# Performance work log

Hardware: AMD Instinct MI355X
Metric: run time of the kernel (lower is better)

Reference implementation:

```python
import jax, jax.numpy as jnp
import numpy as np


def _consts():
    # Hypercube vertices: itertools.product([-1,1], repeat=n) order => MSB-first bits.
    def verts(nbits):
        idx = np.arange(2 ** nbits)
        return (((idx[:, None] >> np.arange(nbits - 1, -1, -1)[None, :]) & 1) * 2.0 - 1.0).astype(np.float32)

    hexagrams = verts(6)   # (64, 6)
    q2_verts = verts(2)    # (4, 2)
    q3_verts = verts(3)    # (8, 3)

    # Q2 vertex -> group one-hot, _Q2_TO_GROUP = [2, 1, 1, 0]
    q2_to_group = np.zeros((4, 3), dtype=np.float32)
    for v, g in enumerate([2, 1, 1, 0]):
        q2_to_group[v, g] = 1.0

    # Group anchors: ABSTRACT = mean(hex[63], hex[62]), DYNAMIC = mean(hex[19], hex[21]),
    # CONCRETE = mean(hex[0], hex[8]); then L2-normalized.
    anch = np.stack([
        hexagrams[[63, 62]].mean(0),
        hexagrams[[19, 21]].mean(0),
        hexagrams[[0, 8]].mean(0),
    ]).astype(np.float32)
    anch = anch / np.clip(np.linalg.norm(anch, axis=-1, keepdims=True), 1e-12, None)

    # Walsh-Hadamard popcount masks, pre-divided by their sums -> (64, 3) matrix.
    bits = np.array([bin(i).count('1') for i in range(64)], dtype=np.float32)
    wa = (bits >= 5).astype(np.float32)
    wd = (bits == 3).astype(np.float32)
    wc = (bits <= 1).astype(np.float32)
    wht_mat = np.stack([wa / wa.sum(), wd / wd.sum(), wc / wc.sum()], axis=1)

    return tuple(jnp.asarray(a) for a in (hexagrams, q2_verts, q3_verts, q2_to_group, anch, wht_mat))


def _q3_to_group_init():
    q3_map = np.zeros((8, 3), dtype=np.float32)
    for i in range(8):
        yc = bin(i).count('1')
        if yc == 0:
            q3_map[i, 2] = 1.0
        elif yc == 1:
            q3_map[i, 1] = 1.0
        elif yc == 2:
            q3_map[i, 0] = 0.6
            q3_map[i, 1] = 0.4
        else:
            q3_map[i, 0] = 1.0
    q3_map = q3_map / np.clip(q3_map.sum(axis=1, keepdims=True), 1e-8, None)
    return q3_map


def setup_inputs() -> dict:
    key = jax.random.key(0)
    k_x, k2, k3, k6 = jax.random.split(key, 4)
    B, T, D = 4, 4096, 2048
    s = 1.0 / float(np.sqrt(D))  # torch Linear default init range
    return {
        'x': jax.random.normal(k_x, (B, T, D), dtype=jnp.float32),
        'ln_w': jnp.ones((D,), dtype=jnp.float32),
        'ln_b': jnp.zeros((D,), dtype=jnp.float32),
        'w_q2': jax.random.uniform(k2, (2, D), minval=-s, maxval=s, dtype=jnp.float32),
        'w_q3': jax.random.uniform(k3, (3, D), minval=-s, maxval=s, dtype=jnp.float32),
        'w_q6': jax.random.uniform(k6, (6, D), minval=-s, maxval=s, dtype=jnp.float32),
        'log_temp': jnp.asarray(np.log(0.5), dtype=jnp.float32),
        'log_scale_mix': jnp.zeros((3,), dtype=jnp.float32),
        'q3_to_group': jnp.asarray(_q3_to_group_init()),
        'log_wht_mix': jnp.asarray(-2.0, dtype=jnp.float32),
    }


def _forward(x, ln_w, ln_b, w_q2, w_q3, w_q6, log_temp, log_scale_mix, q3_to_group, log_wht_mix):
    hexa, q2v, q3v, q2g, anch, wht_mat = _consts()

    # LayerNorm (eps = 1e-5, torch default)
    mu = x.mean(-1, keepdims=True)
    var = ((x - mu) ** 2).mean(-1, keepdims=True)
    h = (x - mu) * jax.lax.rsqrt(var + 1e-5) * ln_w + ln_b

    temp = jnp.clip(jnp.exp(log_temp), 0.1, 5.0)

    # Q2 scale: (B,T,2) -> 4 vertices -> 3 groups
    w2 = jax.nn.softmax(jnp.tanh(h @ w_q2.T) @ q2v.T / temp, axis=-1)
    score_q2 = w2 @ q2g

    # Q3 scale: (B,T,3) -> 8 vertices -> learned soft group map
    w3 = jax.nn.softmax(jnp.tanh(h @ w_q3.T) @ q3v.T / temp, axis=-1)
    score_q3 = w3 @ jax.nn.softmax(q3_to_group, axis=-1)

    # Q6 scale: (B,T,6) -> 64 hexagram vertices
    hex_w = jax.nn.softmax(jnp.tanh(h @ w_q6.T) @ hexa.T / temp, axis=-1)
    score_cos = (hex_w @ hexa) @ anch.T            # cosine-sim vs normalized anchors
    score_wht = hex_w @ wht_mat                    # popcount-mask averages
    alpha = jax.nn.sigmoid(log_wht_mix)
    score_q6 = (1.0 - alpha) * score_cos + alpha * score_wht

    mix = jax.nn.softmax(log_scale_mix)
    group_w = jax.nn.softmax(mix[0] * score_q2 + mix[1] * score_q3 + mix[2] * score_q6, axis=-1)

    mg = group_w.mean(axis=(0, 1))
    mh = hex_w.mean(axis=(0, 1))
    lb_loss = jnp.sum(mg * jnp.log(mg + 1e-8)) + 0.1 * jnp.sum(mh * jnp.log(mh + 1e-8))
    return group_w, hex_w, lb_loss


def reference(x, ln_w, ln_b, w_q2, w_q3, w_q6, log_temp, log_scale_mix, q3_to_group, log_wht_mix):
    return _forward(x, ln_w, ln_b, w_q2, w_q3, w_q6, log_temp, log_scale_mix, q3_to_group, log_wht_mix)
```

## Files before the change

kernel.cpp:

```cpp
#include <hip/hip_runtime.h>
#include <math.h>
#include <string.h>

#define D 2048
#define NTOK 16384
#define NROW 11
#define MROWS_U32 (NROW * D / 2)
#define K1_BLOCKS 1024
#define K1_THREADS 256
#define WSTRIDE_U 1036
#define TILE_S 20

#define WS_A 0
#define WS_B 16
#define WS_IT 32
#define WS_ALPHA 33
#define WS_MIX 34
#define WS_M3 40
#define WS_MERGED 64
#define WS_PART (WS_MERGED + MROWS_U32)

typedef __fp16 h2 __attribute__((ext_vector_type(2)));
typedef __fp16 h8 __attribute__((ext_vector_type(8)));
typedef float f32x4 __attribute__((ext_vector_type(4)));

__device__ __forceinline__ float wsum(float v){
#pragma unroll
  for (int m = 1; m < 64; m <<= 1) v += __shfl_xor(v, m, 64);
  return v;
}
__device__ __forceinline__ float wmax(float v){
#pragma unroll
  for (int m = 1; m < 64; m <<= 1) v = fmaxf(v, __shfl_xor(v, m, 64));
  return v;
}
__device__ __forceinline__ float rcp_fast(float x){ return __builtin_amdgcn_rcpf(x); }
__device__ __forceinline__ float tanh_fast(float x){
  float e = __expf(2.0f * x);
  return 1.0f - 2.0f * rcp_fast(e + 1.0f);
}
__device__ __forceinline__ float sload(const float* __restrict__ p){
  return __uint_as_float(__builtin_amdgcn_readfirstlane(__float_as_uint(*p)));
}
__device__ __forceinline__ unsigned int h2u(h2 h){ unsigned int u; memcpy(&u, &h, 4); return u; }

__global__ __launch_bounds__(256) void k0_prep(
    const float* __restrict__ ln_w, const float* __restrict__ ln_b,
    const float* __restrict__ w_q2, const float* __restrict__ w_q3,
    const float* __restrict__ w_q6,
    const float* __restrict__ log_temp, const float* __restrict__ log_scale_mix,
    const float* __restrict__ q3_to_group, const float* __restrict__ log_wht_mix,
    float* __restrict__ ws)
{
  const int tid = threadIdx.x;
  const int k = blockIdx.x;
  unsigned int* wsu = (unsigned int*)ws;
  if (k < NROW){
    const float* row = (k < 2) ? (w_q2 + (size_t)k * D)
                     : (k < 5) ? (w_q3 + (size_t)(k - 2) * D)
                               : (w_q6 + (size_t)(k - 5) * D);
    float pa = 0.f, pb = 0.f;
    for (int i = tid * 2; i < D; i += 512){
      float w0 = row[i], w1 = row[i + 1];
      h2 h = __builtin_amdgcn_cvt_pkrtz(ln_w[i] * w0, ln_w[i + 1] * w1);
      pa += (float)h[0] + (float)h[1];
      pb = fmaf(ln_b[i], w0, pb);
      pb = fmaf(ln_b[i + 1], w1, pb);
      wsu[WS_MERGED + k * 1024 + i / 2] = h2u(h);
    }
    __shared__ float red[8];
    pa = wsum(pa); pb = wsum(pb);
    if ((tid & 63) == 0){ red[tid >> 6] = pa; red[4 + (tid >> 6)] = pb; }
    __syncthreads();
    if (tid == 0){
      ws[WS_A + k] = red[0] + red[1] + red[2] + red[3];
      ws[WS_B + k] = red[4] + red[5] + red[6] + red[7];
    }
  } else if (tid < 64){
    const int lane = tid;
    float q3v = (lane < 24) ? q3_to_group[lane]   : 0.f;
    float sc  = (lane < 3)  ? log_scale_mix[lane] : 0.f;
    float lt  = (lane == 0) ? log_temp[0]         : 0.f;
    float lw  = (lane == 0) ? log_wht_mix[0]      : 0.f;

    if (lane == 0){
      float t = __expf(lt);
      t = fminf(fmaxf(t, 0.1f), 5.0f);
      ws[WS_IT] = 1.0f / t;
      ws[WS_ALPHA] = 1.0f / (1.0f + __expf(-lw));
    }
    float m0 = __shfl(sc, 0, 64), m1 = __shfl(sc, 1, 64), m2 = __shfl(sc, 2, 64);
    if (lane < 3){
      float mm = fmaxf(m0, fmaxf(m1, m2));
      float e0 = __expf(m0 - mm), e1 = __expf(m1 - mm), e2 = __expf(m2 - mm);
      float inv = 1.0f / (e0 + e1 + e2);
      ws[WS_MIX + lane] = ((lane == 0) ? e0 : (lane == 1) ? e1 : e2) * inv;
    }
    if (lane < 24){
      int r = lane / 3, c = lane - r * 3;
      float v0 = __shfl(q3v, r*3 + 0, 64);
      float v1 = __shfl(q3v, r*3 + 1, 64);
      float v2 = __shfl(q3v, r*3 + 2, 64);
      float mx = fmaxf(v0, fmaxf(v1, v2));
      float f0 = __expf(v0 - mx), f1 = __expf(v1 - mx), f2 = __expf(v2 - mx);
      float iv = 1.0f / (f0 + f1 + f2);
      ws[WS_M3 + lane] = ((c == 0) ? f0 : (c == 1) ? f1 : f2) * iv;
    }
  }
}

__global__ __launch_bounds__(256) void k1_main(
    const float* __restrict__ x, const float* __restrict__ ws,
    float* __restrict__ gout, float* __restrict__ hout, float* __restrict__ part)
{
  __shared__ unsigned int sW[NROW * WSTRIDE_U];
  __shared__ float tile[4][16][TILE_S];
  __shared__ float lred[4][68];
  const int tid  = threadIdx.x;
  const int lane = tid & 63;
  const int wid  = tid >> 6;
  const int blk  = blockIdx.x;
  const int tok0 = blk * 16;
  const int n = lane & 15;
  const int q = lane >> 4;

  const float* xp = x + (size_t)(tok0 + n) * D + wid * 512 + q * 8;

  float4 xa[16];
#pragma unroll
  for (int s = 0; s < 8; ++s){
    xa[2*s]     = *(const float4*)(xp + s * 32);
    xa[2*s + 1] = *(const float4*)(xp + s * 32 + 4);
  }

  {
    const uint4* src = (const uint4*)((const unsigned int*)ws + WS_MERGED);
#pragma unroll
    for (int j = 0; j < 11; ++j){
      int idx = tid + j * 256;
      int r = idx >> 8, i = idx & 255;
      *(uint4*)(sW + r * WSTRIDE_U + i * 4) = src[r * 256 + i];
    }
  }

  float sq = 0.f;
  h8 hxA[8], hxB[8];
#pragma unroll
  for (int s = 0; s < 8; ++s){
    float4 f0 = xa[2*s], f1 = xa[2*s + 1];
    sq = fmaf(f0.x,f0.x, fmaf(f0.y,f0.y, fmaf(f0.z,f0.z, fmaf(f0.w,f0.w, sq))));
    sq = fmaf(f1.x,f1.x, fmaf(f1.y,f1.y, fmaf(f1.z,f1.z, fmaf(f1.w,f1.w, sq))));
    h2 p0 = __builtin_amdgcn_cvt_pkrtz(f0.x, f0.y);
    h2 p1 = __builtin_amdgcn_cvt_pkrtz(f0.z, f0.w);
    h2 p2 = __builtin_amdgcn_cvt_pkrtz(f1.x, f1.y);
    h2 p3 = __builtin_amdgcn_cvt_pkrtz(f1.z, f1.w);
    h8 A;
    A[0]=p0[0]; A[1]=p0[1]; A[2]=p1[0]; A[3]=p1[1];
    A[4]=p2[0]; A[5]=p2[1]; A[6]=p3[0]; A[7]=p3[1];
    hxA[s] = A;
  }

  __syncthreads();

#pragma unroll
  for (int s = 0; s < 8; ++s){
    xa[2*s]     = *(const float4*)(xp + (s + 8) * 32);
    xa[2*s + 1] = *(const float4*)(xp + (s + 8) * 32 + 4);
  }

  const int wr = (n < NROW) ? n : (n - NROW);
  const bool is_ones = (n == NROW);
  const uint4 ones4 = make_uint4(0x3C003C00u, 0x3C003C00u, 0x3C003C00u, 0x3C003C00u);
  const unsigned int* wb = sW + wr * WSTRIDE_U + wid * 256 + q * 4;

  f32x4 acc = {0.f, 0.f, 0.f, 0.f};

#pragma unroll
  for (int s = 0; s < 8; ++s){
    uint4 wq = *(const uint4*)(wb + s * 16);
    if (is_ones) wq = ones4;
    h8 B; memcpy(&B, &wq, 16);
    acc = __builtin_amdgcn_mfma_f32_16x16x32_f16(hxA[s], B, acc, 0, 0, 0);
  }

#pragma unroll
  for (int s = 0; s < 8; ++s){
    float4 f0 = xa[2*s], f1 = xa[2*s + 1];
    sq = fmaf(f0.x,f0.x, fmaf(f0.y,f0.y, fmaf(f0.z,f0.z, fmaf(f0.w,f0.w, sq))));
    sq = fmaf(f1.x,f1.x, fmaf(f1.y,f1.y, fmaf(f1.z,f1.z, fmaf(f1.w,f1.w, sq))));
    h2 p0 = __builtin_amdgcn_cvt_pkrtz(f0.x, f0.y);
    h2 p1 = __builtin_amdgcn_cvt_pkrtz(f0.z, f0.w);
    h2 p2 = __builtin_amdgcn_cvt_pkrtz(f1.x, f1.y);
    h2 p3 = __builtin_amdgcn_cvt_pkrtz(f1.z, f1.w);
    h8 A;
    A[0]=p0[0]; A[1]=p0[1]; A[2]=p1[0]; A[3]=p1[1];
    A[4]=p2[0]; A[5]=p2[1]; A[6]=p3[0]; A[7]=p3[1];
    hxB[s] = A;
  }

#pragma unroll
  for (int s = 0; s < 8; ++s){
    uint4 wq = *(const uint4*)(wb + (s + 8) * 16);
    if (is_ones) wq = ones4;
    h8 B; memcpy(&B, &wq, 16);
    acc = __builtin_amdgcn_mfma_f32_16x16x32_f16(hxB[s], B, acc, 0, 0, 0);
  }

  sq += __shfl_xor(sq, 16, 64);
  sq += __shfl_xor(sq, 32, 64);

#pragma unroll
  for (int r = 0; r < 4; ++r) tile[wid][q * 4 + r][n] = acc[r];
  if (lane < 16) tile[wid][lane][16] = sq;

  __syncthreads();

  float a[NROW], bb[NROW];
#pragma unroll
  for (int k = 0; k < NROW; ++k){ a[k] = sload(ws + WS_A + k); bb[k] = sload(ws + WS_B + k); }
  const float it    = sload(ws + WS_IT);
  const float alpha = sload(ws + WS_ALPHA);
  const float mix0 = sload(ws + WS_MIX), mix1 = sload(ws + WS_MIX + 1), mix2 = sload(ws + WS_MIX + 2);
  float M3r[8][3];
#pragma unroll
  for (int r = 0; r < 8; ++r){
#pragma unroll
    for (int g = 0; g < 3; ++g) M3r[r][g] = sload(ws + WS_M3 + r*3 + g);
  }

  float sgn[6];
#pragma unroll
  for (int j = 0; j < 6; ++j) sgn[j] = ((lane >> (5 - j)) & 1) ? 1.0f : -1.0f;
  const float C5 = 0.44721359549995793f;
  const float A0c[6] = { C5,  C5,  C5,  C5,  C5, 0.f };
  const float A1c[6] = {-0.5f, 0.5f, -0.5f, 0.f, 0.f, 0.5f};
  const float A2c[6] = {-C5, -C5, 0.f, -C5, -C5, -C5};
  float cs0 = 0.f, cs1 = 0.f, cs2 = 0.f;
#pragma unroll
  for (int j = 0; j < 6; ++j){
    cs0 = fmaf(sgn[j], A0c[j], cs0);
    cs1 = fmaf(sgn[j], A1c[j], cs1);
    cs2 = fmaf(sgn[j], A2c[j], cs2);
  }
  const int pc = __popc(lane);
  const float w7c = 1.0f / 7.0f;
  float wh0 = (pc >= 5) ? w7c  : 0.f;
  float wh1 = (pc == 3) ? 0.05f: 0.f;
  float wh2 = (pc <= 1) ? w7c  : 0.f;
  const float m60 = (1.f - alpha)*cs0 + alpha*wh0;
  const float m61 = (1.f - alpha)*cs1 + alpha*wh1;
  const float m62 = (1.f - alpha)*cs2 + alpha*wh2;

  float hsum = 0.f, ga0 = 0.f, ga1 = 0.f, ga2 = 0.f;

#pragma unroll
  for (int i = 0; i < 4; ++i){
    const int tl  = wid * 4 + i;
    const int tok = tok0 + tl;

    float t[12]; float sqv = 0.f;
#pragma unroll
    for (int k = 0; k < 12; ++k) t[k] = 0.f;
#pragma unroll
    for (int hh = 0; hh < 4; ++hh){
      const float* row = &tile[hh][tl][0];
      float4 c0 = *(const float4*)(row);
      float4 c1 = *(const float4*)(row + 4);
      float4 c2 = *(const float4*)(row + 8);
      t[0] += c0.x; t[1] += c0.y; t[2]  += c0.z; t[3]  += c0.w;
      t[4] += c1.x; t[5] += c1.y; t[6]  += c1.z; t[7]  += c1.w;
      t[8] += c2.x; t[9] += c2.y; t[10] += c2.z; t[11] += c2.w;
      sqv += row[16];
    }

    float mean = t[11] * (1.0f / D);
    float var  = fmaf(sqv, 1.0f / D, -mean * mean);
    float rr   = rsqrtf(var + 1e-5f);
    float u[NROW];
#pragma unroll
    for (int k = 0; k < NROW; ++k){
      float d = fmaf(-mean, a[k], t[k]);
      u[k] = tanh_fast(fmaf(rr, d, bb[k]));
    }

    float p01 = u[0] + u[1], m01 = u[0] - u[1];
    float l0 = -p01*it, l1 = -m01*it, l2 = m01*it, l3 = p01*it;
    float mx2 = fmaxf(fmaxf(l0, l1), fmaxf(l2, l3));
    float e0 = __expf(l0-mx2), e1 = __expf(l1-mx2), e2 = __expf(l2-mx2), e3 = __expf(l3-mx2);
    float i2 = rcp_fast(e0 + e1 + e2 + e3);
    float s2g0 = e3 * i2, s2g1 = (e1 + e2) * i2, s2g2 = e0 * i2;

    float l3v[8]; float mx3 = -1e30f;
#pragma unroll
    for (int v = 0; v < 8; ++v){
      float acc3 = ((v & 4) ? u[2] : -u[2]) + ((v & 2) ? u[3] : -u[3]) + ((v & 1) ? u[4] : -u[4]);
      l3v[v] = acc3 * it;
      mx3 = fmaxf(mx3, l3v[v]);
    }
    float w3v[8]; float se3 = 0.f;
#pragma unroll
    for (int v = 0; v < 8; ++v){ w3v[v] = __expf(l3v[v] - mx3); se3 += w3v[v]; }
    float i3 = rcp_fast(se3);
    float s3g0 = 0.f, s3g1 = 0.f, s3g2 = 0.f;
#pragma unroll
    for (int v = 0; v < 8; ++v){
      s3g0 = fmaf(w3v[v], M3r[v][0], s3g0);
      s3g1 = fmaf(w3v[v], M3r[v][1], s3g1);
      s3g2 = fmaf(w3v[v], M3r[v][2], s3g2);
    }
    s3g0 *= i3; s3g1 *= i3; s3g2 *= i3;

    float lg = 0.f;
#pragma unroll
    for (int jj = 0; jj < 6; ++jj) lg = fmaf(sgn[jj], u[5 + jj], lg);
    lg *= it;
    float mx6 = wmax(lg);
    float p   = __expf(lg - mx6);
    float se6 = wsum(p);
    float hw  = p * rcp_fast(se6);
    hout[(size_t)tok * 64 + lane] = hw;
    hsum += hw;
    float s6g0 = wsum(hw * m60);
    float s6g1 = wsum(hw * m61);
    float s6g2 = wsum(hw * m62);

    float g0 = mix0*s2g0 + mix1*s3g0 + mix2*s6g0;
    float g1 = mix0*s2g1 + mix1*s3g1 + mix2*s6g1;
    float g2 = mix0*s2g2 + mix1*s3g2 + mix2*s6g2;
    float gm = fmaxf(g0, fmaxf(g1, g2));
    float y0 = __expf(g0-gm), y1 = __expf(g1-gm), y2 = __expf(g2-gm);
    float gi = rcp_fast(y0 + y1 + y2);
    float gw0 = y0*gi, gw1 = y1*gi, gw2 = y2*gi;
    ga0 += gw0; ga1 += gw1; ga2 += gw2;
    if (lane < 3){
      float val = (lane == 0) ? gw0 : (lane == 1) ? gw1 : gw2;
      gout[(size_t)tok * 3 + lane] = val;
    }
  }

  lred[wid][lane] = hsum;
  if (lane < 3){
    float val = (lane == 0) ? ga0 : (lane == 1) ? ga1 : ga2;
    lred[wid][64 + lane] = val;
  }
  __syncthreads();
  if (tid < 67){
    float v = lred[0][tid] + lred[1][tid] + lred[2][tid] + lred[3][tid];
    part[(size_t)tid * K1_BLOCKS + blk] = v;
  }
}

__global__ __launch_bounds__(1024) void k2_loss(const float* __restrict__ part,
                                                float* __restrict__ lout)
{
  __shared__ float sums[68];
  const int tid = threadIdx.x;
  const int lane = tid & 63;
  const int wid  = tid >> 6;
  for (int jv = wid; jv < 67; jv += 16){
    const float4* p = (const float4*)(part + (size_t)jv * K1_BLOCKS);
    float v = 0.f;
#pragma unroll
    for (int b = 0; b < K1_BLOCKS / 256; ++b){
      float4 q = p[lane + b * 64];
      v += (q.x + q.y) + (q.z + q.w);
    }
    v = wsum(v);
    if (lane == 0) sums[jv] = v;
  }
  __syncthreads();
  if (wid == 0){
    const float inv = 1.0f / (float)NTOK;
    float mh = sums[lane] * inv;
    float term = 0.1f * mh * logf(mh + 1e-8f);
    if (lane < 3){
      float mg = sums[64 + lane] * inv;
      term += mg * logf(mg + 1e-8f);
    }
    float L = wsum(term);
    if (lane == 0) lout[0] = L;
  }
}

extern "C" void kernel_launch(void* const* d_in, const int* in_sizes, int n_in,
                              void* d_out, int out_size, void* d_ws, size_t ws_size,
                              hipStream_t stream)
{
  const float* x             = (const float*)d_in[0];
  const float* ln_w          = (const float*)d_in[1];
  const float* ln_b          = (const float*)d_in[2];
  const float* w_q2          = (const float*)d_in[3];
  const float* w_q3          = (const float*)d_in[4];
  const float* w_q6          = (const float*)d_in[5];
  const float* log_temp      = (const float*)d_in[6];
  const float* log_scale_mix = (const float*)d_in[7];
  const float* q3_to_group   = (const float*)d_in[8];
  const float* log_wht_mix   = (const float*)d_in[9];

  float* out  = (float*)d_out;
  float* gout = out;
  float* hout = out + (size_t)NTOK * 3;
  float* lout = out + (size_t)NTOK * 3 + (size_t)NTOK * 64;
  float* ws   = (float*)d_ws;

  k0_prep<<<12, 256, 0, stream>>>(ln_w, ln_b, w_q2, w_q3, w_q6,
                                  log_temp, log_scale_mix, q3_to_group, log_wht_mix, ws);
  k1_main<<<K1_BLOCKS, K1_THREADS, 0, stream>>>(x, ws, gout, hout, ws + WS_PART);
  k2_loss<<<1, 1024, 0, stream>>>(ws + WS_PART, lout);
}
```

Measured before the change: 46.58 us.

## Process four tokens per wave in parallel and reduce loss partials via atomics

The epilogue now assigns each 16-lane group of a wave to one token, with each lane handling four hexagram vertices, instead of looping over four tokens with full 64-lane reductions. This replaces the serial per-token loop and its 64-wide shuffle reductions with 16-wide ones, and writes hex weights as float4. Loss partial sums are accumulated with atomicAdd into 16 striped sets, which k0 zeroes, so the final kernel shrinks to one wave. The costs are atomic contention on the sets and a dependency on k0 zeroing the accumulators before k1 runs.

```diff
diff --git a/kernel.cpp b/kernel.cpp
--- a/kernel.cpp
+++ b/kernel.cpp
@@ -10,6 +10,7 @@
 #define K1_THREADS 256
 #define WSTRIDE_U 1036
 #define TILE_S 20
+#define NSET 16
 
 #define WS_A 0
 #define WS_B 16
@@ -18,7 +19,7 @@
 #define WS_MIX 34
 #define WS_M3 40
 #define WS_MERGED 64
-#define WS_PART (WS_MERGED + MROWS_U32)
+#define WS_ACC (WS_MERGED + MROWS_U32)
 
 typedef __fp16 h2 __attribute__((ext_vector_type(2)));
 typedef __fp16 h8 __attribute__((ext_vector_type(8)));
@@ -29,9 +30,14 @@
   for (int m = 1; m < 64; m <<= 1) v += __shfl_xor(v, m, 64);
   return v;
 }
-__device__ __forceinline__ float wmax(float v){
-#pragma unroll
-  for (int m = 1; m < 64; m <<= 1) v = fmaxf(v, __shfl_xor(v, m, 64));
+__device__ __forceinline__ float gsum(float v){
+#pragma unroll
+  for (int m = 1; m < 16; m <<= 1) v += __shfl_xor(v, m, 64);
+  return v;
+}
+__device__ __forceinline__ float gmax(float v){
+#pragma unroll
+  for (int m = 1; m < 16; m <<= 1) v = fmaxf(v, __shfl_xor(v, m, 64));
   return v;
 }
 __device__ __forceinline__ float rcp_fast(float x){ return __builtin_amdgcn_rcpf(x); }
@@ -106,16 +112,19 @@
       float iv = 1.0f / (f0 + f1 + f2);
       ws[WS_M3 + lane] = ((c == 0) ? f0 : (c == 1) ? f1 : f2) * iv;
     }
+  } else {
+    for (int i = tid - 64; i < 67 * NSET; i += 192) ws[WS_ACC + i] = 0.f;
   }
 }
 
 __global__ __launch_bounds__(256) void k1_main(
     const float* __restrict__ x, const float* __restrict__ ws,
-    float* __restrict__ gout, float* __restrict__ hout, float* __restrict__ part)
+    float* __restrict__ gout, float* __restrict__ hout, float* __restrict__ accp)
 {
   __shared__ unsigned int sW[NROW * WSTRIDE_U];
   __shared__ float tile[4][16][TILE_S];
-  __shared__ float lred[4][68];
+  __shared__ float4 lredh4[4][16];
+  __shared__ float lredg[4][3];
   const int tid  = threadIdx.x;
   const int lane = tid & 63;
   const int wid  = tid >> 6;
@@ -225,161 +234,174 @@
 #pragma unroll
   for (int r = 0; r < 8; ++r){
 #pragma unroll
-    for (int g = 0; g < 3; ++g) M3r[r][g] = sload(ws + WS_M3 + r*3 + g);
-  }
-
-  float sgn[6];
-#pragma unroll
-  for (int j = 0; j < 6; ++j) sgn[j] = ((lane >> (5 - j)) & 1) ? 1.0f : -1.0f;
+    for (int g2 = 0; g2 < 3; ++g2) M3r[r][g2] = sload(ws + WS_M3 + r*3 + g2);
+  }
+
+  const int g  = lane >> 4;
+  const int l  = lane & 15;
+  const int tl  = wid * 4 + g;
+  const int tok = tok0 + tl;
+
   const float C5 = 0.44721359549995793f;
   const float A0c[6] = { C5,  C5,  C5,  C5,  C5, 0.f };
   const float A1c[6] = {-0.5f, 0.5f, -0.5f, 0.f, 0.f, 0.5f};
   const float A2c[6] = {-C5, -C5, 0.f, -C5, -C5, -C5};
-  float cs0 = 0.f, cs1 = 0.f, cs2 = 0.f;
-#pragma unroll
-  for (int j = 0; j < 6; ++j){
-    cs0 = fmaf(sgn[j], A0c[j], cs0);
-    cs1 = fmaf(sgn[j], A1c[j], cs1);
-    cs2 = fmaf(sgn[j], A2c[j], cs2);
-  }
-  const int pc = __popc(lane);
   const float w7c = 1.0f / 7.0f;
-  float wh0 = (pc >= 5) ? w7c  : 0.f;
-  float wh1 = (pc == 3) ? 0.05f: 0.f;
-  float wh2 = (pc <= 1) ? w7c  : 0.f;
-  const float m60 = (1.f - alpha)*cs0 + alpha*wh0;
-  const float m61 = (1.f - alpha)*cs1 + alpha*wh1;
-  const float m62 = (1.f - alpha)*cs2 + alpha*wh2;
-
-  float hsum = 0.f, ga0 = 0.f, ga1 = 0.f, ga2 = 0.f;
-
-#pragma unroll
-  for (int i = 0; i < 4; ++i){
-    const int tl  = wid * 4 + i;
-    const int tok = tok0 + tl;
-
-    float t[12]; float sqv = 0.f;
-#pragma unroll
-    for (int k = 0; k < 12; ++k) t[k] = 0.f;
-#pragma unroll
-    for (int hh = 0; hh < 4; ++hh){
-      const float* row = &tile[hh][tl][0];
-      float4 c0 = *(const float4*)(row);
-      float4 c1 = *(const float4*)(row + 4);
-      float4 c2 = *(const float4*)(row + 8);
-      t[0] += c0.x; t[1] += c0.y; t[2]  += c0.z; t[3]  += c0.w;
-      t[4] += c1.x; t[5] += c1.y; t[6]  += c1.z; t[7]  += c1.w;
-      t[8] += c2.x; t[9] += c2.y; t[10] += c2.z; t[11] += c2.w;
-      sqv += row[16];
-    }
-
-    float mean = t[11] * (1.0f / D);
-    float var  = fmaf(sqv, 1.0f / D, -mean * mean);
-    float rr   = rsqrtf(var + 1e-5f);
-    float u[NROW];
-#pragma unroll
-    for (int k = 0; k < NROW; ++k){
-      float d = fmaf(-mean, a[k], t[k]);
-      u[k] = tanh_fast(fmaf(rr, d, bb[k]));
-    }
-
-    float p01 = u[0] + u[1], m01 = u[0] - u[1];
-    float l0 = -p01*it, l1 = -m01*it, l2 = m01*it, l3 = p01*it;
-    float mx2 = fmaxf(fmaxf(l0, l1), fmaxf(l2, l3));
-    float e0 = __expf(l0-mx2), e1 = __expf(l1-mx2), e2 = __expf(l2-mx2), e3 = __expf(l3-mx2);
-    float i2 = rcp_fast(e0 + e1 + e2 + e3);
-    float s2g0 = e3 * i2, s2g1 = (e1 + e2) * i2, s2g2 = e0 * i2;
-
-    float l3v[8]; float mx3 = -1e30f;
-#pragma unroll
-    for (int v = 0; v < 8; ++v){
-      float acc3 = ((v & 4) ? u[2] : -u[2]) + ((v & 2) ? u[3] : -u[3]) + ((v & 1) ? u[4] : -u[4]);
-      l3v[v] = acc3 * it;
-      mx3 = fmaxf(mx3, l3v[v]);
-    }
-    float w3v[8]; float se3 = 0.f;
-#pragma unroll
-    for (int v = 0; v < 8; ++v){ w3v[v] = __expf(l3v[v] - mx3); se3 += w3v[v]; }
-    float i3 = rcp_fast(se3);
-    float s3g0 = 0.f, s3g1 = 0.f, s3g2 = 0.f;
-#pragma unroll
-    for (int v = 0; v < 8; ++v){
-      s3g0 = fmaf(w3v[v], M3r[v][0], s3g0);
-      s3g1 = fmaf(w3v[v], M3r[v][1], s3g1);
-      s3g2 = fmaf(w3v[v], M3r[v][2], s3g2);
-    }
-    s3g0 *= i3; s3g1 *= i3; s3g2 *= i3;
-
-    float lg = 0.f;
-#pragma unroll
-    for (int jj = 0; jj < 6; ++jj) lg = fmaf(sgn[jj], u[5 + jj], lg);
-    lg *= it;
-    float mx6 = wmax(lg);
-    float p   = __expf(lg - mx6);
-    float se6 = wsum(p);
-    float hw  = p * rcp_fast(se6);
-    hout[(size_t)tok * 64 + lane] = hw;
-    hsum += hw;
-    float s6g0 = wsum(hw * m60);
-    float s6g1 = wsum(hw * m61);
-    float s6g2 = wsum(hw * m62);
-
-    float g0 = mix0*s2g0 + mix1*s3g0 + mix2*s6g0;
-    float g1 = mix0*s2g1 + mix1*s3g1 + mix2*s6g1;
-    float g2 = mix0*s2g2 + mix1*s3g2 + mix2*s6g2;
-    float gm = fmaxf(g0, fmaxf(g1, g2));
-    float y0 = __expf(g0-gm), y1 = __expf(g1-gm), y2 = __expf(g2-gm);
-    float gi = rcp_fast(y0 + y1 + y2);
-    float gw0 = y0*gi, gw1 = y1*gi, gw2 = y2*gi;
-    ga0 += gw0; ga1 += gw1; ga2 += gw2;
-    if (lane < 3){
-      float val = (lane == 0) ? gw0 : (lane == 1) ? gw1 : gw2;
-      gout[(size_t)tok * 3 + lane] = val;
-    }
-  }
-
-  lred[wid][lane] = hsum;
+  float m60v[4], m61v[4], m62v[4];
+#pragma unroll
+  for (int j = 0; j < 4; ++j){
+    const int v = l * 4 + j;
+    float cs0 = 0.f, cs1 = 0.f, cs2 = 0.f;
+#pragma unroll
+    for (int jj = 0; jj < 6; ++jj){
+      float s = ((v >> (5 - jj)) & 1) ? 1.0f : -1.0f;
+      cs0 = fmaf(s, A0c[jj], cs0);
+      cs1 = fmaf(s, A1c[jj], cs1);
+      cs2 = fmaf(s, A2c[jj], cs2);
+    }
+    const int pcv = __popc(v);
+    float wh0 = (pcv >= 5) ? w7c  : 0.f;
+    float wh1 = (pcv == 3) ? 0.05f: 0.f;
+    float wh2 = (pcv <= 1) ? w7c  : 0.f;
+    m60v[j] = (1.f - alpha)*cs0 + alpha*wh0;
+    m61v[j] = (1.f - alpha)*cs1 + alpha*wh1;
+    m62v[j] = (1.f - alpha)*cs2 + alpha*wh2;
+  }
+
+  float t[12]; float sqv = 0.f;
+#pragma unroll
+  for (int k = 0; k < 12; ++k) t[k] = 0.f;
+#pragma unroll
+  for (int hh = 0; hh < 4; ++hh){
+    const float* row = &tile[hh][tl][0];
+    float4 c0 = *(const float4*)(row);
+    float4 c1 = *(const float4*)(row + 4);
+    float4 c2 = *(const float4*)(row + 8);
+    t[0] += c0.x; t[1] += c0.y; t[2]  += c0.z; t[3]  += c0.w;
+    t[4] += c1.x; t[5] += c1.y; t[6]  += c1.z; t[7]  += c1.w;
+    t[8] += c2.x; t[9] += c2.y; t[10] += c2.z; t[11] += c2.w;
+    sqv += row[16];
+  }
+
+  float mean = t[11] * (1.0f / D);
+  float var  = fmaf(sqv, 1.0f / D, -mean * mean);
+  float rr   = rsqrtf(var + 1e-5f);
+  float u[NROW];
+#pragma unroll
+  for (int k = 0; k < NROW; ++k){
+    float d = fmaf(-mean, a[k], t[k]);
+    u[k] = tanh_fast(fmaf(rr, d, bb[k]));
+  }
+
+  float p01 = u[0] + u[1], m01 = u[0] - u[1];
+  float l0 = -p01*it, l1 = -m01*it, l2 = m01*it, l3 = p01*it;
+  float mx2 = fmaxf(fmaxf(l0, l1), fmaxf(l2, l3));
+  float e0 = __expf(l0-mx2), e1 = __expf(l1-mx2), e2 = __expf(l2-mx2), e3 = __expf(l3-mx2);
+  float i2 = rcp_fast(e0 + e1 + e2 + e3);
+  float s2g0 = e3 * i2, s2g1 = (e1 + e2) * i2, s2g2 = e0 * i2;
+
+  float l3v[8]; float mx3 = -1e30f;
+#pragma unroll
+  for (int v = 0; v < 8; ++v){
+    float acc3 = ((v & 4) ? u[2] : -u[2]) + ((v & 2) ? u[3] : -u[3]) + ((v & 1) ? u[4] : -u[4]);
+    l3v[v] = acc3 * it;
+    mx3 = fmaxf(mx3, l3v[v]);
+  }
+  float w3v[8]; float se3 = 0.f;
+#pragma unroll
+  for (int v = 0; v < 8; ++v){ w3v[v] = __expf(l3v[v] - mx3); se3 += w3v[v]; }
+  float i3 = rcp_fast(se3);
+  float s3g0 = 0.f, s3g1 = 0.f, s3g2 = 0.f;
+#pragma unroll
+  for (int v = 0; v < 8; ++v){
+    s3g0 = fmaf(w3v[v], M3r[v][0], s3g0);
+    s3g1 = fmaf(w3v[v], M3r[v][1], s3g1);
+    s3g2 = fmaf(w3v[v], M3r[v][2], s3g2);
+  }
+  s3g0 *= i3; s3g1 *= i3; s3g2 *= i3;
+
+  float lg[4];
+#pragma unroll
+  for (int j = 0; j < 4; ++j){
+    const int v = l * 4 + j;
+    float acc6 = 0.f;
+#pragma unroll
+    for (int jj = 0; jj < 6; ++jj)
+      acc6 += ((v >> (5 - jj)) & 1) ? u[5 + jj] : -u[5 + jj];
+    lg[j] = acc6 * it;
+  }
+  float mx6 = fmaxf(fmaxf(lg[0], lg[1]), fmaxf(lg[2], lg[3]));
+  mx6 = gmax(mx6);
+  float p6[4]; float se6 = 0.f;
+#pragma unroll
+  for (int j = 0; j < 4; ++j){ p6[j] = __expf(lg[j] - mx6); se6 += p6[j]; }
+  se6 = gsum(se6);
+  float inv6 = rcp_fast(se6);
+  float hw0 = p6[0]*inv6, hw1 = p6[1]*inv6, hw2 = p6[2]*inv6, hw3 = p6[3]*inv6;
+  *(float4*)(hout + (size_t)tok * 64 + l * 4) = make_float4(hw0, hw1, hw2, hw3);
+  float s6g0 = gsum(fmaf(hw0,m60v[0], fmaf(hw1,m60v[1], fmaf(hw2,m60v[2], hw3*m60v[3]))));
+  float s6g1 = gsum(fmaf(hw0,m61v[0], fmaf(hw1,m61v[1], fmaf(hw2,m61v[2], hw3*m61v[3]))));
+  float s6g2 = gsum(fmaf(hw0,m62v[0], fmaf(hw1,m62v[1], fmaf(hw2,m62v[2], hw3*m62v[3]))));
+
+  float g0 = mix0*s2g0 + mix1*s3g0 + mix2*s6g0;
+  float g1 = mix0*s2g1 + mix1*s3g1 + mix2*s6g1;
+  float g2 = mix0*s2g2 + mix1*s3g2 + mix2*s6g2;
+  float gm = fmaxf(g0, fmaxf(g1, g2));
+  float y0 = __expf(g0-gm), y1 = __expf(g1-gm), y2 = __expf(g2-gm);
+  float gi = rcp_fast(y0 + y1 + y2);
+  float gw0 = y0*gi, gw1 = y1*gi, gw2 = y2*gi;
+  if (l < 3){
+    float val = (l == 0) ? gw0 : (l == 1) ? gw1 : gw2;
+    gout[(size_t)tok * 3 + l] = val;
+  }
+
+  float h0 = hw0, h1 = hw1, h2 = hw2, h3 = hw3;
+  h0 += __shfl_xor(h0, 16, 64); h0 += __shfl_xor(h0, 32, 64);
+  h1 += __shfl_xor(h1, 16, 64); h1 += __shfl_xor(h1, 32, 64);
+  h2 += __shfl_xor(h2, 16, 64); h2 += __shfl_xor(h2, 32, 64);
+  h3 += __shfl_xor(h3, 16, 64); h3 += __shfl_xor(h3, 32, 64);
+  float ga0 = gw0, ga1 = gw1, ga2 = gw2;
+  ga0 += __shfl_xor(ga0, 16, 64); ga0 += __shfl_xor(ga0, 32, 64);
+  ga1 += __shfl_xor(ga1, 16, 64); ga1 += __shfl_xor(ga1, 32, 64);
+  ga2 += __shfl_xor(ga2, 16, 64); ga2 += __shfl_xor(ga2, 32, 64);
+  if (g == 0){
+    lredh4[wid][l] = make_float4(h0, h1, h2, h3);
+    if (l == 0){ lredg[wid][0] = ga0; lredg[wid][1] = ga1; lredg[wid][2] = ga2; }
+  }
+  __syncthreads();
+  const int set = blk & (NSET - 1);
+  if (tid < 64){
+    const float* lh = (const float*)&lredh4[0][0];
+    float v = lh[tid] + lh[64 + tid] + lh[128 + tid] + lh[192 + tid];
+    atomicAdd(&accp[tid * NSET + set], v);
+  } else if (tid < 67){
+    int gg = tid - 64;
+    float v = lredg[0][gg] + lredg[1][gg] + lredg[2][gg] + lredg[3][gg];
+    atomicAdd(&accp[tid * NSET + set], v);
+  }
+}
+
+__global__ __launch_bounds__(64) void k2_loss(const float* __restrict__ accp,
+                                              float* __restrict__ lout)
+{
+  const int lane = threadIdx.x;
+  const float4* ap = (const float4*)(accp + lane * NSET);
+  float4 a0 = ap[0], a1 = ap[1], a2 = ap[2], a3 = ap[3];
+  float s = (a0.x+a0.y+a0.z+a0.w) + (a1.x+a1.y+a1.z+a1.w)
+          + (a2.x+a2.y+a2.z+a2.w) + (a3.x+a3.y+a3.z+a3.w);
+  const float inv = 1.0f / (float)NTOK;
+  float mh = s * inv;
+  float term = 0.1f * mh * logf(mh + 1e-8f);
   if (lane < 3){
-    float val = (lane == 0) ? ga0 : (lane == 1) ? ga1 : ga2;
-    lred[wid][64 + lane] = val;
-  }
-  __syncthreads();
-  if (tid < 67){
-    float v = lred[0][tid] + lred[1][tid] + lred[2][tid] + lred[3][tid];
-    part[(size_t)tid * K1_BLOCKS + blk] = v;
-  }
-}
-
-__global__ __launch_bounds__(1024) void k2_loss(const float* __restrict__ part,
-                                                float* __restrict__ lout)
-{
-  __shared__ float sums[68];
-  const int tid = threadIdx.x;
-  const int lane = tid & 63;
-  const int wid  = tid >> 6;
-  for (int jv = wid; jv < 67; jv += 16){
-    const float4* p = (const float4*)(part + (size_t)jv * K1_BLOCKS);
-    float v = 0.f;
-#pragma unroll
-    for (int b = 0; b < K1_BLOCKS / 256; ++b){
-      float4 q = p[lane + b * 64];
-      v += (q.x + q.y) + (q.z + q.w);
-    }
-    v = wsum(v);
-    if (lane == 0) sums[jv] = v;
-  }
-  __syncthreads();
-  if (wid == 0){
-    const float inv = 1.0f / (float)NTOK;
-    float mh = sums[lane] * inv;
-    float term = 0.1f * mh * logf(mh + 1e-8f);
-    if (lane < 3){
-      float mg = sums[64 + lane] * inv;
-      term += mg * logf(mg + 1e-8f);
-    }
-    float L = wsum(term);
-    if (lane == 0) lout[0] = L;
-  }
+    const float* gp = accp + (64 + lane) * NSET;
+    float sg = 0.f;
+#pragma unroll
+    for (int i = 0; i < NSET; ++i) sg += gp[i];
+    float mg = sg * inv;
+    term += mg * logf(mg + 1e-8f);
+  }
+  float L = wsum(term);
+  if (lane == 0) lout[0] = L;
 }
 
 extern "C" void kernel_launch(void* const* d_in, const int* in_sizes, int n_in,
@@ -405,6 +427,6 @@
 
   k0_prep<<<12, 256, 0, stream>>>(ln_w, ln_b, w_q2, w_q3, w_q6,
                                   log_temp, log_scale_mix, q3_to_group, log_wht_mix, ws);
-  k1_main<<<K1_BLOCKS, K1_THREADS, 0, stream>>>(x, ws, gout, hout, ws + WS_PART);
-  k2_loss<<<1, 1024, 0, stream>>>(ws + WS_PART, lout);
-}
+  k1_main<<<K1_BLOCKS, K1_THREADS, 0, stream>>>(x, ws, gout, hout, ws + WS_ACC);
+  k2_loss<<<1, 64, 0, stream>>>(ws + WS_ACC, lout);
+}
```

Result: slower. 50.20 us (+7.8%).

## Process two 16-token tiles per block with prefetch of next tile's x

Applied to the files above, without the earlier changes.

Each block now handles 32 tokens in two iterations, halving the grid to 512 blocks, so the 11-row fp16 weight matrix copied into shared memory is loaded half as often per token. The first half of the next tile's x is loaded while the current tile's second MFMA pass runs, overlapping global loads with compute. The cost is an extra barrier per iteration, higher register pressure, and fewer blocks to spread across CUs, which may reduce occupancy and latency hiding.

```diff
diff --git a/kernel.cpp b/kernel.cpp
--- a/kernel.cpp
+++ b/kernel.cpp
@@ -6,7 +6,7 @@
 #define NTOK 16384
 #define NROW 11
 #define MROWS_U32 (NROW * D / 2)
-#define K1_BLOCKS 1024
+#define K1_BLOCKS 512
 #define K1_THREADS 256
 #define WSTRIDE_U 1036
 #define TILE_S 20
@@ -120,17 +120,16 @@
   const int lane = tid & 63;
   const int wid  = tid >> 6;
   const int blk  = blockIdx.x;
-  const int tok0 = blk * 16;
+  const int tokbase = blk * 32;
   const int n = lane & 15;
   const int q = lane >> 4;
 
-  const float* xp = x + (size_t)(tok0 + n) * D + wid * 512 + q * 8;
-
+  const float* xp0 = x + (size_t)(tokbase + n) * D + wid * 512 + q * 8;
   float4 xa[16];
 #pragma unroll
   for (int s = 0; s < 8; ++s){
-    xa[2*s]     = *(const float4*)(xp + s * 32);
-    xa[2*s + 1] = *(const float4*)(xp + s * 32 + 4);
+    xa[2*s]     = *(const float4*)(xp0 + s * 32);
+    xa[2*s + 1] = *(const float4*)(xp0 + s * 32 + 4);
   }
 
   {
@@ -162,59 +161,6 @@
 
   __syncthreads();
 
-#pragma unroll
-  for (int s = 0; s < 8; ++s){
-    xa[2*s]     = *(const float4*)(xp + (s + 8) * 32);
-    xa[2*s + 1] = *(const float4*)(xp + (s + 8) * 32 + 4);
-  }
-
-  const int wr = (n < NROW) ? n : (n - NROW);
-  const bool is_ones = (n == NROW);
-  const uint4 ones4 = make_uint4(0x3C003C00u, 0x3C003C00u, 0x3C003C00u, 0x3C003C00u);
-  const unsigned int* wb = sW + wr * WSTRIDE_U + wid * 256 + q * 4;
-
-  f32x4 acc = {0.f, 0.f, 0.f, 0.f};
-
-#pragma unroll
-  for (int s = 0; s < 8; ++s){
-    uint4 wq = *(const uint4*)(wb + s * 16);
-    if (is_ones) wq = ones4;
-    h8 B; memcpy(&B, &wq, 16);
-    acc = __builtin_amdgcn_mfma_f32_16x16x32_f16(hxA[s], B, acc, 0, 0, 0);
-  }
-
-#pragma unroll
-  for (int s = 0; s < 8; ++s){
-    float4 f0 = xa[2*s], f1 = xa[2*s + 1];
-    sq = fmaf(f0.x,f0.x, fmaf(f0.y,f0.y, fmaf(f0.z,f0.z, fmaf(f0.w,f0.w, sq))));
-    sq = fmaf(f1.x,f1.x, fmaf(f1.y,f1.y, fmaf(f1.z,f1.z, fmaf(f1.w,f1.w, sq))));
-    h2 p0 = __builtin_amdgcn_cvt_pkrtz(f0.x, f0.y);
-    h2 p1 = __builtin_amdgcn_cvt_pkrtz(f0.z, f0.w);
-    h2 p2 = __builtin_amdgcn_cvt_pkrtz(f1.x, f1.y);
-    h2 p3 = __builtin_amdgcn_cvt_pkrtz(f1.z, f1.w);
-    h8 A;
-    A[0]=p0[0]; A[1]=p0[1]; A[2]=p1[0]; A[3]=p1[1];
-    A[4]=p2[0]; A[5]=p2[1]; A[6]=p3[0]; A[7]=p3[1];
-    hxB[s] = A;
-  }
-
-#pragma unroll
-  for (int s = 0; s < 8; ++s){
-    uint4 wq = *(const uint4*)(wb + (s + 8) * 16);
-    if (is_ones) wq = ones4;
-    h8 B; memcpy(&B, &wq, 16);
-    acc = __builtin_amdgcn_mfma_f32_16x16x32_f16(hxB[s], B, acc, 0, 0, 0);
-  }
-
-  sq += __shfl_xor(sq, 16, 64);
-  sq += __shfl_xor(sq, 32, 64);
-
-#pragma unroll
-  for (int r = 0; r < 4; ++r) tile[wid][q * 4 + r][n] = acc[r];
-  if (lane < 16) tile[wid][lane][16] = sq;
-
-  __syncthreads();
-
   float a[NROW], bb[NROW];
 #pragma unroll
   for (int k = 0; k < NROW; ++k){ a[k] = sload(ws + WS_A + k); bb[k] = sload(ws + WS_B + k); }
@@ -225,9 +171,8 @@
 #pragma unroll
   for (int r = 0; r < 8; ++r){
 #pragma unroll
-    for (int g = 0; g < 3; ++g) M3r[r][g] = sload(ws + WS_M3 + r*3 + g);
-  }
-
+    for (int g2 = 0; g2 < 3; ++g2) M3r[r][g2] = sload(ws + WS_M3 + r*3 + g2);
+  }
   float sgn[6];
 #pragma unroll
   for (int j = 0; j < 6; ++j) sgn[j] = ((lane >> (5 - j)) & 1) ? 1.0f : -1.0f;
@@ -251,91 +196,179 @@
   const float m61 = (1.f - alpha)*cs1 + alpha*wh1;
   const float m62 = (1.f - alpha)*cs2 + alpha*wh2;
 
+  const int wr = (n < NROW) ? n : (n - NROW);
+  const bool is_ones = (n == NROW);
+  const uint4 ones4 = make_uint4(0x3C003C00u, 0x3C003C00u, 0x3C003C00u, 0x3C003C00u);
+  const unsigned int* wb = sW + wr * WSTRIDE_U + wid * 256 + q * 4;
+
   float hsum = 0.f, ga0 = 0.f, ga1 = 0.f, ga2 = 0.f;
 
-#pragma unroll
-  for (int i = 0; i < 4; ++i){
-    const int tl  = wid * 4 + i;
-    const int tok = tok0 + tl;
-
-    float t[12]; float sqv = 0.f;
-#pragma unroll
-    for (int k = 0; k < 12; ++k) t[k] = 0.f;
-#pragma unroll
-    for (int hh = 0; hh < 4; ++hh){
-      const float* row = &tile[hh][tl][0];
-      float4 c0 = *(const float4*)(row);
-      float4 c1 = *(const float4*)(row + 4);
-      float4 c2 = *(const float4*)(row + 8);
-      t[0] += c0.x; t[1] += c0.y; t[2]  += c0.z; t[3]  += c0.w;
-      t[4] += c1.x; t[5] += c1.y; t[6]  += c1.z; t[7]  += c1.w;
-      t[8] += c2.x; t[9] += c2.y; t[10] += c2.z; t[11] += c2.w;
-      sqv += row[16];
-    }
-
-    float mean = t[11] * (1.0f / D);
-    float var  = fmaf(sqv, 1.0f / D, -mean * mean);
-    float rr   = rsqrtf(var + 1e-5f);
-    float u[NROW];
-#pragma unroll
-    for (int k = 0; k < NROW; ++k){
-      float d = fmaf(-mean, a[k], t[k]);
-      u[k] = tanh_fast(fmaf(rr, d, bb[k]));
-    }
-
-    float p01 = u[0] + u[1], m01 = u[0] - u[1];
-    float l0 = -p01*it, l1 = -m01*it, l2 = m01*it, l3 = p01*it;
-    float mx2 = fmaxf(fmaxf(l0, l1), fmaxf(l2, l3));
-    float e0 = __expf(l0-mx2), e1 = __expf(l1-mx2), e2 = __expf(l2-mx2), e3 = __expf(l3-mx2);
-    float i2 = rcp_fast(e0 + e1 + e2 + e3);
-    float s2g0 = e3 * i2, s2g1 = (e1 + e2) * i2, s2g2 = e0 * i2;
-
-    float l3v[8]; float mx3 = -1e30f;
-#pragma unroll
-    for (int v = 0; v < 8; ++v){
-      float acc3 = ((v & 4) ? u[2] : -u[2]) + ((v & 2) ? u[3] : -u[3]) + ((v & 1) ? u[4] : -u[4]);
-      l3v[v] = acc3 * it;
-      mx3 = fmaxf(mx3, l3v[v]);
-    }
-    float w3v[8]; float se3 = 0.f;
-#pragma unroll
-    for (int v = 0; v < 8; ++v){ w3v[v] = __expf(l3v[v] - mx3); se3 += w3v[v]; }
-    float i3 = rcp_fast(se3);
-    float s3g0 = 0.f, s3g1 = 0.f, s3g2 = 0.f;
-#pragma unroll
-    for (int v = 0; v < 8; ++v){
-      s3g0 = fmaf(w3v[v], M3r[v][0], s3g0);
-      s3g1 = fmaf(w3v[v], M3r[v][1], s3g1);
-      s3g2 = fmaf(w3v[v], M3r[v][2], s3g2);
-    }
-    s3g0 *= i3; s3g1 *= i3; s3g2 *= i3;
-
-    float lg = 0.f;
-#pragma unroll
-    for (int jj = 0; jj < 6; ++jj) lg = fmaf(sgn[jj], u[5 + jj], lg);
-    lg *= it;
-    float mx6 = wmax(lg);
-    float p   = __expf(lg - mx6);
-    float se6 = wsum(p);
-    float hw  = p * rcp_fast(se6);
-    hout[(size_t)tok * 64 + lane] = hw;
-    hsum += hw;
-    float s6g0 = wsum(hw * m60);
-    float s6g1 = wsum(hw * m61);
-    float s6g2 = wsum(hw * m62);
-
-    float g0 = mix0*s2g0 + mix1*s3g0 + mix2*s6g0;
-    float g1 = mix0*s2g1 + mix1*s3g1 + mix2*s6g1;
-    float g2 = mix0*s2g2 + mix1*s3g2 + mix2*s6g2;
-    float gm = fmaxf(g0, fmaxf(g1, g2));
-    float y0 = __expf(g0-gm), y1 = __expf(g1-gm), y2 = __expf(g2-gm);
-    float gi = rcp_fast(y0 + y1 + y2);
-    float gw0 = y0*gi, gw1 = y1*gi, gw2 = y2*gi;
-    ga0 += gw0; ga1 += gw1; ga2 += gw2;
-    if (lane < 3){
-      float val = (lane == 0) ? gw0 : (lane == 1) ? gw1 : gw2;
-      gout[(size_t)tok * 3 + lane] = val;
-    }
+#pragma unroll 1
+  for (int tt = 0; tt < 2; ++tt){
+    const int tok0 = tokbase + tt * 16;
+    const float* xp = x + (size_t)(tok0 + n) * D + wid * 512 + q * 8;
+
+    if (tt > 0){
+      sq = 0.f;
+#pragma unroll
+      for (int s = 0; s < 8; ++s){
+        float4 f0 = xa[2*s], f1 = xa[2*s + 1];
+        sq = fmaf(f0.x,f0.x, fmaf(f0.y,f0.y, fmaf(f0.z,f0.z, fmaf(f0.w,f0.w, sq))));
+        sq = fmaf(f1.x,f1.x, fmaf(f1.y,f1.y, fmaf(f1.z,f1.z, fmaf(f1.w,f1.w, sq))));
+        h2 p0 = __builtin_amdgcn_cvt_pkrtz(f0.x, f0.y);
+        h2 p1 = __builtin_amdgcn_cvt_pkrtz(f0.z, f0.w);
+        h2 p2 = __builtin_amdgcn_cvt_pkrtz(f1.x, f1.y);
+        h2 p3 = __builtin_amdgcn_cvt_pkrtz(f1.z, f1.w);
+        h8 A;
+        A[0]=p0[0]; A[1]=p0[1]; A[2]=p1[0]; A[3]=p1[1];
+        A[4]=p2[0]; A[5]=p2[1]; A[6]=p3[0]; A[7]=p3[1];
+        hxA[s] = A;
+      }
+    }
+
+#pragma unroll
+    for (int s = 0; s < 8; ++s){
+      xa[2*s]     = *(const float4*)(xp + (s + 8) * 32);
+      xa[2*s + 1] = *(const float4*)(xp + (s + 8) * 32 + 4);
+    }
+
+    f32x4 acc = {0.f, 0.f, 0.f, 0.f};
+#pragma unroll
+    for (int s = 0; s < 8; ++s){
+      uint4 wq = *(const uint4*)(wb + s * 16);
+      if (is_ones) wq = ones4;
+      h8 B; memcpy(&B, &wq, 16);
+      acc = __builtin_amdgcn_mfma_f32_16x16x32_f16(hxA[s], B, acc, 0, 0, 0);
+    }
+
+#pragma unroll
+    for (int s = 0; s < 8; ++s){
+      float4 f0 = xa[2*s], f1 = xa[2*s + 1];
+      sq = fmaf(f0.x,f0.x, fmaf(f0.y,f0.y, fmaf(f0.z,f0.z, fmaf(f0.w,f0.w, sq))));
+      sq = fmaf(f1.x,f1.x, fmaf(f1.y,f1.y, fmaf(f1.z,f1.z, fmaf(f1.w,f1.w, sq))));
+      h2 p0 = __builtin_amdgcn_cvt_pkrtz(f0.x, f0.y);
+      h2 p1 = __builtin_amdgcn_cvt_pkrtz(f0.z, f0.w);
+      h2 p2 = __builtin_amdgcn_cvt_pkrtz(f1.x, f1.y);
+      h2 p3 = __builtin_amdgcn_cvt_pkrtz(f1.z, f1.w);
+      h8 A;
+      A[0]=p0[0]; A[1]=p0[1]; A[2]=p1[0]; A[3]=p1[1];
+      A[4]=p2[0]; A[5]=p2[1]; A[6]=p3[0]; A[7]=p3[1];
+      hxB[s] = A;
+    }
+
+    if (tt == 0){
+      const float* xpn = x + (size_t)(tok0 + 16 + n) * D + wid * 512 + q * 8;
+#pragma unroll
+      for (int s = 0; s < 8; ++s){
+        xa[2*s]     = *(const float4*)(xpn + s * 32);
+        xa[2*s + 1] = *(const float4*)(xpn + s * 32 + 4);
+      }
+    }
+
+#pragma unroll
+    for (int s = 0; s < 8; ++s){
+      uint4 wq = *(const uint4*)(wb + (s + 8) * 16);
+      if (is_ones) wq = ones4;
+      h8 B; memcpy(&B, &wq, 16);
+      acc = __builtin_amdgcn_mfma_f32_16x16x32_f16(hxB[s], B, acc, 0, 0, 0);
+    }
+
+    float sqr = sq;
+    sqr += __shfl_xor(sqr, 16, 64);
+    sqr += __shfl_xor(sqr, 32, 64);
+
+#pragma unroll
+    for (int r = 0; r < 4; ++r) tile[wid][q * 4 + r][n] = acc[r];
+    if (lane < 16) tile[wid][lane][16] = sqr;
+
+    __syncthreads();
+
+#pragma unroll
+    for (int i = 0; i < 4; ++i){
+      const int tl  = wid * 4 + i;
+      const int tok = tok0 + tl;
+
+      float t[12]; float sqv = 0.f;
+#pragma unroll
+      for (int k = 0; k < 12; ++k) t[k] = 0.f;
+#pragma unroll
+      for (int hh = 0; hh < 4; ++hh){
+        const float* row = &tile[hh][tl][0];
+        float4 c0 = *(const float4*)(row);
+        float4 c1 = *(const float4*)(row + 4);
+        float4 c2 = *(const float4*)(row + 8);
+        t[0] += c0.x; t[1] += c0.y; t[2]  += c0.z; t[3]  += c0.w;
+        t[4] += c1.x; t[5] += c1.y; t[6]  += c1.z; t[7]  += c1.w;
+        t[8] += c2.x; t[9] += c2.y; t[10] += c2.z; t[11] += c2.w;
+        sqv += row[16];
+      }
+
+      float mean = t[11] * (1.0f / D);
+      float var  = fmaf(sqv, 1.0f / D, -mean * mean);
+      float rr   = rsqrtf(var + 1e-5f);
+      float u[NROW];
+#pragma unroll
+      for (int k = 0; k < NROW; ++k){
+        float d = fmaf(-mean, a[k], t[k]);
+        u[k] = tanh_fast(fmaf(rr, d, bb[k]));
+      }
+
+      float p01 = u[0] + u[1], m01 = u[0] - u[1];
+      float l0 = -p01*it, l1 = -m01*it, l2 = m01*it, l3 = p01*it;
+      float mx2 = fmaxf(fmaxf(l0, l1), fmaxf(l2, l3));
+      float e0 = __expf(l0-mx2), e1 = __expf(l1-mx2), e2 = __expf(l2-mx2), e3 = __expf(l3-mx2);
+      float i2 = rcp_fast(e0 + e1 + e2 + e3);
+      float s2g0 = e3 * i2, s2g1 = (e1 + e2) * i2, s2g2 = e0 * i2;
+
+      float l3v[8]; float mx3 = -1e30f;
+#pragma unroll
+      for (int v = 0; v < 8; ++v){
+        float acc3 = ((v & 4) ? u[2] : -u[2]) + ((v & 2) ? u[3] : -u[3]) + ((v & 1) ? u[4] : -u[4]);
+        l3v[v] = acc3 * it;
+        mx3 = fmaxf(mx3, l3v[v]);
+      }
+      float w3v[8]; float se3 = 0.f;
+#pragma unroll
+      for (int v = 0; v < 8; ++v){ w3v[v] = __expf(l3v[v] - mx3); se3 += w3v[v]; }
+      float i3 = rcp_fast(se3);
+      float s3g0 = 0.f, s3g1 = 0.f, s3g2 = 0.f;
+#pragma unroll
+      for (int v = 0; v < 8; ++v){
+        s3g0 = fmaf(w3v[v], M3r[v][0], s3g0);
+        s3g1 = fmaf(w3v[v], M3r[v][1], s3g1);
+        s3g2 = fmaf(w3v[v], M3r[v][2], s3g2);
+      }
+      s3g0 *= i3; s3g1 *= i3; s3g2 *= i3;
+
+      float lg = 0.f;
+#pragma unroll
+      for (int jj = 0; jj < 6; ++jj) lg = fmaf(sgn[jj], u[5 + jj], lg);
+      lg *= it;
+      float mx6 = wmax(lg);
+      float p   = __expf(lg - mx6);
+      float se6 = wsum(p);
+      float hw  = p * rcp_fast(se6);
+      hout[(size_t)tok * 64 + lane] = hw;
+      hsum += hw;
+      float s6g0 = wsum(hw * m60);
+      float s6g1 = wsum(hw * m61);
+      float s6g2 = wsum(hw * m62);
+
+      float g0 = mix0*s2g0 + mix1*s3g0 + mix2*s6g0;
+      float g1 = mix0*s2g1 + mix1*s3g1 + mix2*s6g1;
+      float g2 = mix0*s2g2 + mix1*s3g2 + mix2*s6g2;
+      float gm = fmaxf(g0, fmaxf(g1, g2));
+      float y0 = __expf(g0-gm), y1 = __expf(g1-gm), y2 = __expf(g2-gm);
+      float gi = rcp_fast(y0 + y1 + y2);
+      float gw0 = y0*gi, gw1 = y1*gi, gw2 = y2*gi;
+      ga0 += gw0; ga1 += gw1; ga2 += gw2;
+      if (lane < 3){
+        float val = (lane == 0) ? gw0 : (lane == 1) ? gw1 : gw2;
+        gout[(size_t)tok * 3 + lane] = val;
+      }
+    }
+
+    __syncthreads();
   }
 
   lred[wid][lane] = hsum;
```

New measurement: 49.23 us. +5.7%, slower.
